# Optimization experiments

Measured on AMD Instinct MI355X. Metric: run time of the kernel, lower is better.

## Reference

```python
import jax, jax.numpy as jnp
import numpy as np

B, NPG = 32, 512            # graphs, nodes per graph
N = B * NPG                  # total nodes
EPG = 4096                   # edges per graph
E = B * EPG                  # total edges
H = 4                        # attention heads
IN, HID, OUT = 512, 128, 64
K1, K2 = 308, 185            # ceil(0.6*512), ceil(0.6*308) -- SAGPooling ratio=0.6
SLOPE = 0.2                  # GATv2 leaky_relu negative slope


def _segment_softmax(logit, seg, num_seg):
    # numerically stable softmax over edges grouped by destination node
    m = jax.ops.segment_max(logit, seg, num_segments=num_seg)
    m = jnp.where(jnp.isfinite(m), m, 0.0)
    ex = jnp.exp(logit - m[seg])
    s = jax.ops.segment_sum(ex, seg, num_segments=num_seg)
    return ex / (s[seg] + 1e-16)


def _gatv2(x, src, dst, valid, Wl, bl, Wr, br, att, bias, n):
    # PyG GATv2Conv, heads=H, concat=False (head-mean), add_self_loops=True,
    # attention dropout (0.2) is a no-op in eval mode.
    h, c = att.shape
    xl = (x @ Wl + bl).reshape(n, h, c)
    xr = (x @ Wr + br).reshape(n, h, c)
    loops = jnp.arange(n, dtype=src.dtype)
    sa = jnp.concatenate([src, loops])
    da = jnp.concatenate([dst, loops])
    va = jnp.concatenate([valid, jnp.ones((n,), bool)])
    seg = jnp.where(va, da, n)  # invalid edges -> dummy segment n
    e = jax.nn.leaky_relu(xl[sa] + xr[da], SLOPE)      # [Ea,h,c]
    logit = jnp.einsum('ehc,hc->eh', e, att)            # [Ea,h]
    alpha = _segment_softmax(logit, seg, n + 1)
    msg = alpha[:, :, None] * xl[sa]
    out = jax.ops.segment_sum(msg, seg, num_segments=n + 1)[:n]
    return out.mean(axis=1) + bias


def _sage_score(x, src, dst, valid, Wn, Wr, b, n):
    # PyG SAGEConv (mean aggr, root weight), out_channels=1 -> pooling score
    seg = jnp.where(valid, dst, n)
    vf = valid[:, None].astype(x.dtype)
    s = jax.ops.segment_sum(x[src] * vf, seg, num_segments=n + 1)[:n]
    cnt = jax.ops.segment_sum(valid.astype(x.dtype), seg, num_segments=n + 1)[:n]
    mean = s / jnp.maximum(cnt, 1.0)[:, None]
    return (mean @ Wn + x @ Wr + b).squeeze(-1)


def _pool(x, src, dst, valid, score, n_old, k):
    # SAGPooling top-k per graph (equal-sized graphs -> static k), tanh gating,
    # then filter_adj: keep edges whose endpoints both survive (mask + reindex).
    npg = n_old // B
    _, topi = jax.lax.top_k(score.reshape(B, npg), k)
    perm = (topi + (jnp.arange(B) * npg)[:, None]).reshape(-1)
    x_new = x[perm] * jnp.tanh(score[perm])[:, None]
    n_new = B * k
    nmap = jnp.full((n_old,), -1, src.dtype).at[perm].set(jnp.arange(n_new, dtype=src.dtype))
    ns, nd = nmap[src], nmap[dst]
    v = valid & (ns >= 0) & (nd >= 0)
    return x_new, jnp.where(v, ns, 0), jnp.where(v, nd, 0), v, n_new


def _gmp(x):
    # global max pool; nodes are grouped contiguously, equal count per graph
    return x.reshape(B, -1, x.shape[-1]).max(axis=1)


def _forward(x_feat, Wl1, bl1, Wr1, br1, att1, bias1,
             Wl2, bl2, Wr2, br2, att2, bias2,
             Wsn, Wsr, bs, Wf, bf, edge_index):
    src, dst = edge_index[0], edge_index[1]
    valid = jnp.ones((E,), bool)
    x = jax.nn.relu(_gatv2(x_feat, src, dst, valid, Wl1, bl1, Wr1, br1, att1, bias1, N))
    x1 = _gmp(x)
    sc = _sage_score(x, src, dst, valid, Wsn, Wsr, bs, N)
    x, s2, d2, v2, n2 = _pool(x, src, dst, valid, sc, N, K1)
    x2 = _gmp(x)
    x = jax.nn.relu(_gatv2(x, s2, d2, v2, Wl2, bl2, Wr2, br2, att2, bias2, n2))
    sc = _sage_score(x, s2, d2, v2, Wsn, Wsr, bs, n2)
    x, s3, d3, v3, n3 = _pool(x, s2, d2, v2, sc, n2, K2)
    x3 = _gmp(x)
    x = x1 + x2 + x3
    return jax.nn.relu(x @ Wf + bf)


def setup_inputs() -> dict:
    key = jax.random.key(0)
    ks = jax.random.split(key, 12)
    x_feat = jax.random.normal(ks[0], (N, IN), jnp.float32)
    sl = jax.random.randint(ks[1], (B, EPG), 0, NPG)
    dl = jax.random.randint(ks[2], (B, EPG), 0, NPG)
    off = (jnp.arange(B) * NPG)[:, None]
    edge_index = jnp.stack([(sl + off).reshape(-1), (dl + off).reshape(-1)])
    batch = jnp.repeat(jnp.arange(B), NPG)
    g = lambda k, shape, fan: jax.random.normal(k, shape, jnp.float32) / np.sqrt(fan).astype(np.float32)
    z = lambda shape: jnp.zeros(shape, jnp.float32)
    return dict(
        x_feat=x_feat, edge_index=edge_index, batch=batch,
        Wl1=g(ks[3], (IN, H * HID), IN), bl1=z((H * HID,)),
        Wr1=g(ks[4], (IN, H * HID), IN), br1=z((H * HID,)),
        att1=g(ks[5], (H, HID), HID), bias1=z((HID,)),
        Wl2=g(ks[6], (HID, H * HID), HID), bl2=z((H * HID,)),
        Wr2=g(ks[7], (HID, H * HID), HID), br2=z((H * HID,)),
        att2=g(ks[8], (H, HID), HID), bias2=z((HID,)),
        Wsn=g(ks[9], (HID, 1), HID), Wsr=g(ks[10], (HID, 1), HID), bs=z((1,)),
        Wf=g(ks[11], (HID, OUT), HID), bf=z((OUT,)),
    )


def reference(x_feat, edge_index, batch,
              Wl1, bl1, Wr1, br1, att1, bias1,
              Wl2, bl2, Wr2, br2, att2, bias2,
              Wsn, Wsr, bs, Wf, bf):
    # batch is implied by the contiguous equal-size grouping used above
    return _forward(x_feat, Wl1, bl1, Wr1, br1, att1, bias1,
                    Wl2, bl2, Wr2, br2, att2, bias2,
                    Wsn, Wsr, bs, Wf, bf, edge_index)
```

## Files before the change

### kernel.cpp

```cpp
#include <hip/hip_runtime.h>
#include <hip/hip_bf16.h>
#include <math.h>

#define NB    32
#define NPG   512
#define NTOT  (NB*NPG)
#define EPG   4096
#define ETOT  (NB*EPG)
#define K1    308
#define K2    185
#define N2    (NB*K1)
#define N3    (NB*K2)
#define SLOPE 0.2f

typedef _Float16 f16;
typedef f16   f16x8 __attribute__((ext_vector_type(8)));
typedef float f32x4 __attribute__((ext_vector_type(4)));

#define WSCALE 512.0f
#define WINV   (1.0f/512.0f)

__device__ __forceinline__ unsigned enc_f(float v) {
    unsigned u = __float_as_uint(v);
    return (u & 0x80000000u) ? ~u : (u | 0x80000000u);
}
__device__ __forceinline__ float dec_f(unsigned e) {
    return (e & 0x80000000u) ? __uint_as_float(e ^ 0x80000000u) : __uint_as_float(~e);
}

__device__ __forceinline__ void gll16(const void* g, void* l)
{
    __builtin_amdgcn_global_load_lds(
        (const __attribute__((address_space(1))) unsigned int*)g,
        (__attribute__((address_space(3))) unsigned int*)l, 16, 0, 0);
}


__global__ __launch_bounds__(256) void split_a(const float* __restrict__ A,
                                               f16* __restrict__ Ah, f16* __restrict__ Al,
                                               int K8, unsigned* __restrict__ xg,
                                               int* __restrict__ cnt)
{
    __shared__ float tile[64][65];
    int t = threadIdx.x;
    int kx = blockIdx.x, ry = blockIdx.y;
    int gid = (ry * gridDim.x + kx) * 256 + t;
    if (gid < 3 * NB * 128) xg[gid] = 0u;
    if (gid >= 16384 && gid < 16384 + NTOT + 8) cnt[gid - 16384] = 0;

    int K = K8 * 8;
    int r = t >> 2, q = t & 3;
    const float* src = A + (size_t)(ry * 64 + r) * K + kx * 64 + q * 16;
#pragma unroll
    for (int i = 0; i < 4; ++i) {
        float4 v = *(const float4*)(src + i * 4);
        tile[r][q * 16 + i * 4 + 0] = v.x;
        tile[r][q * 16 + i * 4 + 1] = v.y;
        tile[r][q * 16 + i * 4 + 2] = v.z;
        tile[r][q * 16 + i * 4 + 3] = v.w;
    }
    __syncthreads();
    int rr = t & 63, kb0 = t >> 6;
#pragma unroll
    for (int kk = 0; kk < 2; ++kk) {
        int kb = kb0 + kk * 4;
        f16x8 h, l;
#pragma unroll
        for (int c = 0; c < 8; ++c) {
            float v = tile[rr][kb * 8 + c];
            f16 hh = (f16)v;
            h[c] = hh;
            l[c] = (f16)(v - (float)hh);
        }
        size_t off = (((size_t)ry * K8 + kx * 8 + kb) * 64 + rr) * 8;
        *(f16x8*)(Ah + off) = h;
        *(f16x8*)(Al + off) = l;
    }
}

__global__ __launch_bounds__(256) void prep_w(const float* __restrict__ WL,
                                              const float* __restrict__ WR,
                                              f16* __restrict__ Wh, f16* __restrict__ Wlo,
                                              int K)
{
    __shared__ float t[32][33];
    int bk = blockIdx.x;
    int bn = blockIdx.y;
    int tx = threadIdx.x & 31, ty = threadIdx.x >> 5;
    const float* Wsrc = (bn < 16) ? WL : WR;
    int ncol = bn * 32 - (bn < 16 ? 0 : 512) + tx;
    int K8 = K >> 3;
#pragma unroll
    for (int q = 0; q < 4; ++q) {
        int kk = bk * 32 + ty + q * 8;
        t[ty + q * 8][tx] = Wsrc[(size_t)kk * 512 + ncol];
    }
    __syncthreads();
#pragma unroll
    for (int q = 0; q < 4; ++q) {
        int n = bn * 32 + ty + q * 8;
        int k = bk * 32 + tx;
        float v = t[tx][ty + q * 8] * WSCALE;
        f16 h = (f16)v;
        size_t off = (((size_t)(n >> 6) * K8 + (k >> 3)) * 64 + (n & 63)) * 8 + (k & 7);
        Wh [off] = h;
        Wlo[off] = (f16)(v - (float)h);
    }
}

__global__ __launch_bounds__(256) void gemm_split(
    const f16* __restrict__ Ah, const f16* __restrict__ Al,
    const f16* __restrict__ Bh, const f16* __restrict__ Bl,
    const float* __restrict__ bias_l, const float* __restrict__ bias_r,
    float* __restrict__ XL, float* __restrict__ XR, int M, int K)
{
    __shared__ f16 sm[2][4][4][128][8];
    int tid = threadIdx.x;
    int wave = tid >> 6, lane = tid & 63;

    int l = blockIdx.y * gridDim.x + blockIdx.x;
    int rows = gridDim.y;
    int row0 = (l % rows) * 128, col0 = (l / rows) * 128;

    const f16* base = (wave == 0) ? Ah : (wave == 1) ? Al : (wave == 2) ? Bh : Bl;
    int rc0 = (wave < 2) ? row0 : col0;
    int tr0 = rc0 >> 6;

    int wr = wave >> 1, wc = wave & 1;
    int r16 = lane & 15, kb = lane >> 4;

    const int K8 = K >> 3;
    const int nt = K >> 5;

    auto stage = [&](int buf, int t) {
#pragma unroll
        for (int i = 0; i < 8; ++i) {
            int kblk = i >> 1, rh = i & 1;
            const f16* src = base + ((((size_t)(tr0 + rh)) * K8 + (t * 4 + kblk)) << 9) + lane * 8;
            gll16(src, &sm[buf][wave][kblk][rh * 64][0]);
        }
    };

    f32x4 acc[4][4] = {};
    int cur = 0;
    stage(0, 0);

    for (int t = 0; t < nt; ++t) {
        if (t + 1 < nt) {
            stage(cur ^ 1, t + 1);
            asm volatile("s_waitcnt vmcnt(8)" ::: "memory");
        } else {
            asm volatile("s_waitcnt vmcnt(0)" ::: "memory");
        }
        __builtin_amdgcn_s_barrier();

        f16x8 a_h[4], a_l[4], b_h[4], b_l[4];
#pragma unroll
        for (int m = 0; m < 4; ++m) {
            a_h[m] = *(const f16x8*)&sm[cur][0][kb][wr * 64 + m * 16 + r16][0];
            a_l[m] = *(const f16x8*)&sm[cur][1][kb][wr * 64 + m * 16 + r16][0];
        }
#pragma unroll
        for (int n = 0; n < 4; ++n) {
            b_h[n] = *(const f16x8*)&sm[cur][2][kb][wc * 64 + n * 16 + r16][0];
            b_l[n] = *(const f16x8*)&sm[cur][3][kb][wc * 64 + n * 16 + r16][0];
        }
#pragma unroll
        for (int m = 0; m < 4; ++m)
#pragma unroll
            for (int n = 0; n < 4; ++n)
                acc[m][n] = __builtin_amdgcn_mfma_f32_16x16x32_f16(a_h[m], b_h[n], acc[m][n], 0, 0, 0);
#pragma unroll
        for (int m = 0; m < 4; ++m)
#pragma unroll
            for (int n = 0; n < 4; ++n)
                acc[m][n] = __builtin_amdgcn_mfma_f32_16x16x32_f16(a_h[m], b_l[n], acc[m][n], 0, 0, 0);
#pragma unroll
        for (int m = 0; m < 4; ++m)
#pragma unroll
            for (int n = 0; n < 4; ++n)
                acc[m][n] = __builtin_amdgcn_mfma_f32_16x16x32_f16(a_l[m], b_h[n], acc[m][n], 0, 0, 0);

        __syncthreads();
        cur ^= 1;
    }
    float* Co = (col0 < 512) ? XL : XR;
    const float* bo = (col0 < 512) ? bias_l : bias_r;
    int cbase = col0 - (col0 < 512 ? 0 : 512);
#pragma unroll
    for (int m = 0; m < 4; ++m)
#pragma unroll
        for (int n = 0; n < 4; ++n) {
            int cc = cbase + wc * 64 + n * 16 + r16;
            float b = bo[cc];
#pragma unroll
            for (int j = 0; j < 4; ++j) {
                int rr = row0 + wr * 64 + m * 16 + kb * 4 + j;
                Co[(size_t)rr * 512 + cc] = acc[m][n][j] * WINV + b;
            }
        }
}

__global__ void count_edges(const int* __restrict__ dst, int E_in, int* __restrict__ cnt)
{
    int e = blockIdx.x * blockDim.x + threadIdx.x;
    if (e < E_in) atomicAdd(&cnt[dst[e]], 1);
}

__global__ void fill_edges(const int* __restrict__ src, const int* __restrict__ dst,
                           int E_in, int* __restrict__ next, int* __restrict__ csr)
{
    int e = blockIdx.x * blockDim.x + threadIdx.x;
    if (e < E_in) {
        int p = atomicAdd(&next[dst[e]], 1);
        csr[p] = src[e];
    }
}

__global__ __launch_bounds__(512) void scan_graph(const int* __restrict__ cnt,
                                                  int* __restrict__ off, int* __restrict__ next)
{
    __shared__ int s[512];
    int g = blockIdx.x, t = threadIdx.x;
    int node = g * NPG + t;
    int v = cnt[node];
    s[t] = v;
    __syncthreads();
    for (int d = 1; d < 512; d <<= 1) {
        int u = (t >= d) ? s[t - d] : 0;
        __syncthreads();
        s[t] += u;
        __syncthreads();
    }
    int excl = s[t] - v + g * EPG;
    off[node] = excl;
    next[node] = excl;
    if (g == NB - 1 && t == 511) off[NTOT] = ETOT;
}

__global__ __launch_bounds__(64) void graph_sums(const int* __restrict__ cnt,
                                                 int* __restrict__ gsum)
{
    int b = blockIdx.x, t = threadIdx.x;
    int s = 0;
    for (int i = t; i < K1; i += 64) s += cnt[b * K1 + i];
#pragma unroll
    for (int sh = 1; sh < 64; sh <<= 1) s += __shfl_xor(s, sh);
    if (t == 0) gsum[b] = s;
}

__global__ __launch_bounds__(512) void scan_graph2(const int* __restrict__ cnt,
                                                   const int* __restrict__ gsum,
                                                   int* __restrict__ off, int* __restrict__ next)
{
    __shared__ int s[512];
    __shared__ int sbase;
    int b = blockIdx.x, t = threadIdx.x;
    if (t < 64) {
        int v = (t < b) ? gsum[t] : 0;
#pragma unroll
        for (int sh = 1; sh < 64; sh <<= 1) v += __shfl_xor(v, sh);
        if (t == 0) sbase = v;
    }
    int node = b * K1 + t;
    int c = (t < K1) ? cnt[node] : 0;
    s[t] = c;
    __syncthreads();
    for (int d = 1; d < 512; d <<= 1) {
        int u = (t >= d) ? s[t - d] : 0;
        __syncthreads();
        s[t] += u;
        __syncthreads();
    }
    int excl = sbase + s[t] - c;
    if (t < K1) { off[node] = excl; next[node] = excl; }
    if (b == NB - 1 && t == K1 - 1) off[N2] = excl + c;
}

__global__ void remap_edges(const int* __restrict__ src, const int* __restrict__ dst,
                            int E_in, const int* __restrict__ nmap,
                            int* __restrict__ es2, int* __restrict__ ed2,
                            int* __restrict__ ec2, int* __restrict__ cnt2)
{
    int e = blockIdx.x * blockDim.x + threadIdx.x;
    if (e >= E_in) return;
    int ns = nmap[src[e]], nd = nmap[dst[e]];
    if (ns >= 0 && nd >= 0) {
        int pos = atomicAdd(ec2, 1);
        es2[pos] = ns; ed2[pos] = nd;
        atomicAdd(&cnt2[nd], 1);
    }
}

__global__ void fill_edges_dyn(const int* __restrict__ es, const int* __restrict__ ed,
                               const int* __restrict__ ec, int* __restrict__ next,
                               int* __restrict__ csr)
{
    int e = blockIdx.x * blockDim.x + threadIdx.x;
    if (e < *ec) {
        int p = atomicAdd(&next[ed[e]], 1);
        csr[p] = es[e];
    }
}

__global__ __launch_bounds__(256) void gatv2_agg(
    const float* __restrict__ XL, const float* __restrict__ XR,
    const int* __restrict__ csr_src, const int* __restrict__ off,
    const float* __restrict__ att, const float* __restrict__ bias,
    const float* __restrict__ Wn, const float* __restrict__ Wr,
    float* __restrict__ out, float* __restrict__ y, float* __restrict__ z,
    int n, unsigned* __restrict__ xgOut, int npg, int* __restrict__ zc)
{
    __shared__ float hb[4][128];
    if (zc) {
        int raw = blockIdx.x * 256 + threadIdx.x;
        if (raw < NTOT + 2) zc[raw] = 0;
    }
    int nwg = gridDim.x;
    int q = nwg >> 3;
    int swz = (blockIdx.x & 7) * q + (blockIdx.x >> 3);
    int wv = threadIdx.x >> 6;
    int wid = swz * 4 + wv;
    int lane = threadIdx.x & 63;
    if (wid >= n) return;
    const int f0 = lane * 8;
    float xr[8], atv[8];
    {
        float4 r0 = *(const float4*)&XR[(size_t)wid * 512 + f0];
        float4 r1 = *(const float4*)&XR[(size_t)wid * 512 + f0 + 4];
        xr[0]=r0.x; xr[1]=r0.y; xr[2]=r0.z; xr[3]=r0.w;
        xr[4]=r1.x; xr[5]=r1.y; xr[6]=r1.z; xr[7]=r1.w;
        float4 t0 = *(const float4*)&att[f0];
        float4 t1 = *(const float4*)&att[f0 + 4];
        atv[0]=t0.x; atv[1]=t0.y; atv[2]=t0.z; atv[3]=t0.w;
        atv[4]=t1.x; atv[5]=t1.y; atv[6]=t1.z; atv[7]=t1.w;
    }

    auto loadrow = [&](int s, float* xl) {
        float4 l0 = *(const float4*)&XL[(size_t)s * 512 + f0];
        float4 l1 = *(const float4*)&XL[(size_t)s * 512 + f0 + 4];
        xl[0]=l0.x; xl[1]=l0.y; xl[2]=l0.z; xl[3]=l0.w;
        xl[4]=l1.x; xl[5]=l1.y; xl[6]=l1.z; xl[7]=l1.w;
    };
    auto logit = [&](const float* xl) {
        float part = 0.f;
#pragma unroll
        for (int j = 0; j < 8; ++j) {
            float v = xl[j] + xr[j];
            v = (v > 0.f) ? v : SLOPE * v;
            part += v * atv[j];
        }
        part += __shfl_xor(part, 1);
        part += __shfl_xor(part, 2);
        part += __shfl_xor(part, 4);
        part += __shfl_xor(part, 8);
        return part;
    };

    float xl0[8], acc[8];
    loadrow(wid, xl0);
    float m = logit(xl0), ssum = 1.f;
#pragma unroll
    for (int j = 0; j < 8; ++j) acc[j] = xl0[j];

    int e0 = off[wid], e1 = off[wid + 1];
    int e = e0;
    for (; e + 3 < e1; e += 4) {
        int s1 = csr_src[e], s2 = csr_src[e + 1], s3 = csr_src[e + 2], s4 = csr_src[e + 3];
        float xl1[8], xl2[8], xl3[8], xl4[8];
        loadrow(s1, xl1);
        loadrow(s2, xl2);
        loadrow(s3, xl3);
        loadrow(s4, xl4);
        float p1 = logit(xl1), p2 = logit(xl2), p3 = logit(xl3), p4 = logit(xl4);
        float mx = fmaxf(fmaxf(p1, p2), fmaxf(p3, p4));
        float mn = fmaxf(m, mx);
        float scale = __expf(m - mn);
        float q1 = __expf(p1 - mn), q2 = __expf(p2 - mn);
        float q3 = __expf(p3 - mn), q4 = __expf(p4 - mn);
        ssum = ssum * scale + (q1 + q2 + q3 + q4);
#pragma unroll
        for (int j = 0; j < 8; ++j)
            acc[j] = acc[j] * scale + (q1 * xl1[j] + q2 * xl2[j] + q3 * xl3[j] + q4 * xl4[j]);
        m = mn;
    }
    for (; e < e1; ++e) {
        int s1 = csr_src[e];
        float xl1[8];
        loadrow(s1, xl1);
        float p1 = logit(xl1);
        float mn = fmaxf(m, p1);
        float scale = __expf(m - mn);
        float q1 = __expf(p1 - mn);
        ssum = ssum * scale + q1;
#pragma unroll
        for (int j = 0; j < 8; ++j) acc[j] = acc[j] * scale + q1 * xl1[j];
        m = mn;
    }

    float inv = 1.f / ssum;
    float py = 0.f, pz = 0.f;
#pragma unroll
    for (int j = 0; j < 8; ++j) {
        float v = acc[j] * inv;
        v += __shfl_xor(v, 16);
        v += __shfl_xor(v, 32);
        if (lane < 16) {
            int c = lane * 8 + j;
            float r = fmaxf(0.25f * v + bias[c], 0.f);
            out[(size_t)wid * 128 + c] = r;
            py += r * Wn[c];
            pz += r * Wr[c];
            if (xgOut) hb[wv][c] = r;
        }
    }
#pragma unroll
    for (int sh = 1; sh < 16; sh <<= 1) {
        py += __shfl_xor(py, sh);
        pz += __shfl_xor(pz, sh);
    }
    if (lane == 0) { y[wid] = py; z[wid] = pz; }
    if (xgOut) {
        __syncthreads();
        int t = threadIdx.x;
        if (t < 128) {
            float mx = fmaxf(fmaxf(hb[0][t], hb[1][t]), fmaxf(hb[2][t], hb[3][t]));
            int gb = (swz * 4) / npg;
            atomicMax(&xgOut[gb * 128 + t], enc_f(mx));
        }
    }
}

__global__ __launch_bounds__(512) void sage_rank(
    const float* __restrict__ y, const float* __restrict__ z,
    const int* __restrict__ csr, const int* __restrict__ off,
    const float* __restrict__ bs, int npg, int k,
    float* __restrict__ score, int* __restrict__ nmap)
{
    __shared__ float s[512];
    int b = blockIdx.x, t = threadIdx.x;
    int node = b * npg + t;
    if (t < npg) {
        int e0 = off[node], e1 = off[node + 1];
        float a = 0.f;
        int e = e0;
        for (; e + 3 < e1; e += 4)
            a += y[csr[e]] + y[csr[e + 1]] + y[csr[e + 2]] + y[csr[e + 3]];
        for (; e < e1; ++e) a += y[csr[e]];
        float sc = a / fmaxf((float)(e1 - e0), 1.f) + z[node] + bs[0];
        s[t] = sc;
        score[node] = sc;
    }
    __syncthreads();
    if (t < npg) {
        float mine = s[t];
        int rank = 0;
        for (int j = 0; j < npg; ++j) {
            float v = s[j];
            rank += (v > mine) || (v == mine && j < t);
        }
        nmap[node] = (rank < k) ? (b * k + rank) : -1;
    }
}

__global__ __launch_bounds__(256) void pool_gather(
    const float* __restrict__ X, const float* __restrict__ score,
    const int* __restrict__ nmap, f16* __restrict__ Xh, f16* __restrict__ Xl,
    unsigned* __restrict__ xgOut, int kk, int ntot)
{
    int gid = blockIdx.x * 256 + threadIdx.x;
    int i = gid >> 6, l6 = gid & 63;
    if (i >= ntot) return;
    int nid = nmap[i];
    if (nid < 0) return;
    int c0 = l6 * 2;
    float t = tanhf(score[i]);
    float2 xv = *(const float2*)&X[(size_t)i * 128 + c0];
    float v0 = xv.x * t, v1 = xv.y * t;
    if (Xh) {
        size_t off = (((size_t)(nid >> 6) * 16 + (c0 >> 3)) * 64 + (nid & 63)) * 8 + (c0 & 7);
        f16 h0 = (f16)v0, h1 = (f16)v1;
        Xh[off] = h0;     Xl[off] = (f16)(v0 - (float)h0);
        Xh[off + 1] = h1; Xl[off + 1] = (f16)(v1 - (float)h1);
    }
    int b = nid / kk;
    atomicMax(&xgOut[b * 128 + c0], enc_f(v0));
    atomicMax(&xgOut[b * 128 + c0 + 1], enc_f(v1));
}

__global__ void final_mlp(const unsigned* __restrict__ xg,
                          const float* __restrict__ Wf,
                          const float* __restrict__ bf, float* __restrict__ out)
{
    int b = blockIdx.x, o = threadIdx.x;
    float acc = bf[o];
    for (int c = 0; c < 128; ++c) {
        int i = b * 128 + c;
        float xv = dec_f(xg[i]) + dec_f(xg[4096 + i]) + dec_f(xg[8192 + i]);
        acc += xv * Wf[c * 64 + o];
    }
    out[b * 64 + o] = fmaxf(acc, 0.f);
}

static inline size_t alignup(size_t x) { return (x + 255) & ~(size_t)255; }

extern "C" void kernel_launch(void* const* d_in, const int* in_sizes, int n_in,
                              void* d_out, int out_size, void* d_ws, size_t ws_size,
                              hipStream_t stream)
{
    const float* x_feat = (const float*)d_in[0];
    const int*   ei     = (const int*)d_in[1];
    const float* Wl1  = (const float*)d_in[3];
    const float* bl1  = (const float*)d_in[4];
    const float* Wr1  = (const float*)d_in[5];
    const float* br1  = (const float*)d_in[6];
    const float* att1 = (const float*)d_in[7];
    const float* bias1= (const float*)d_in[8];
    const float* Wl2  = (const float*)d_in[9];
    const float* bl2  = (const float*)d_in[10];
    const float* Wr2  = (const float*)d_in[11];
    const float* br2  = (const float*)d_in[12];
    const float* att2 = (const float*)d_in[13];
    const float* bias2= (const float*)d_in[14];
    const float* Wsn  = (const float*)d_in[15];
    const float* Wsr  = (const float*)d_in[16];
    const float* bs   = (const float*)d_in[17];
    const float* Wf   = (const float*)d_in[18];
    const float* bf   = (const float*)d_in[19];
    float* out = (float*)d_out;

    const int* e_src = ei;
    const int* e_dst = ei + ETOT;

    char* ws = (char*)d_ws;
    size_t o = 0;
    auto take = [&](size_t bytes) { size_t r = o; o = alignup(o + bytes); return r; };
    float* XL   = (float*)(ws + take((size_t)NTOT * 512 * 4));
    float* XR   = (float*)(ws + take((size_t)NTOT * 512 * 4));
    float* H1   = (float*)(ws + take((size_t)NTOT * 128 * 4));
    float* H2   = (float*)(ws + take((size_t)N2 * 128 * 4));
    f16*   Ah1  = (f16*)(ws + take((size_t)NTOT * 512 * 2));
    f16*   Al1  = (f16*)(ws + take((size_t)NTOT * 512 * 2));
    f16*   Wh1  = (f16*)(ws + take((size_t)1024 * 512 * 2));
    f16*   Wo1  = (f16*)(ws + take((size_t)1024 * 512 * 2));
    f16*   Wh2  = (f16*)(ws + take((size_t)1024 * 128 * 2));
    f16*   Wo2  = (f16*)(ws + take((size_t)1024 * 128 * 2));
    f16*   PXh  = (f16*)(ws + take((size_t)N2 * 128 * 2));
    f16*   PXl  = (f16*)(ws + take((size_t)N2 * 128 * 2));
    float* score= (float*)(ws + take((size_t)NTOT * 4));
    float* yb   = (float*)(ws + take((size_t)NTOT * 4));
    float* zb   = (float*)(ws + take((size_t)NTOT * 4));
    int*   nmap = (int*)(ws + take((size_t)NTOT * 4));
    int*   cnt  = (int*)(ws + take((size_t)(NTOT + 1) * 4 + 256));
    int*   offs = (int*)(ws + take((size_t)(NTOT + 1) * 4));
    int*   nxt  = (int*)(ws + take((size_t)(NTOT + 1) * 4));
    int*   gsum = (int*)(ws + take(256));
    int*   csr1 = (int*)(ws + take((size_t)ETOT * 4));
    int*   es2  = (int*)(ws + take((size_t)ETOT * 4));
    int*   ed2  = (int*)(ws + take((size_t)ETOT * 4));
    int*   csr2 = (int*)(ws + take((size_t)ETOT * 4));
    unsigned* xg = (unsigned*)(ws + take((size_t)3 * NB * 128 * 4));
    int* ec2 = cnt + NTOT + 1;
    (void)ws_size; (void)in_sizes; (void)n_in; (void)out_size;

    split_a<<<dim3(8, NTOT / 64), 256, 0, stream>>>(x_feat, Ah1, Al1, 64, xg, cnt);
    prep_w<<<dim3(512 / 32, 32), 256, 0, stream>>>(Wl1, Wr1, Wh1, Wo1, 512);
    prep_w<<<dim3(128 / 32, 32), 256, 0, stream>>>(Wl2, Wr2, Wh2, Wo2, 128);

    gemm_split<<<dim3(8, NTOT / 128), 256, 0, stream>>>(Ah1, Al1, Wh1, Wo1, bl1, br1, XL, XR, NTOT, 512);

    count_edges<<<ETOT / 256, 256, 0, stream>>>(e_dst, ETOT, cnt);
    scan_graph<<<NB, 512, 0, stream>>>(cnt, offs, nxt);
    fill_edges<<<ETOT / 256, 256, 0, stream>>>(e_src, e_dst, ETOT, nxt, csr1);

    gatv2_agg<<<NTOT / 4, 256, 0, stream>>>(XL, XR, csr1, offs, att1, bias1, Wsn, Wsr,
                                            H1, yb, zb, NTOT, xg, NPG, cnt);

    sage_rank<<<NB, 512, 0, stream>>>(yb, zb, csr1, offs, bs, NPG, K1, score, nmap);
    pool_gather<<<NTOT * 64 / 256, 256, 0, stream>>>(H1, score, nmap, PXh, PXl, xg + 4096, K1, NTOT);

    remap_edges<<<ETOT / 256, 256, 0, stream>>>(e_src, e_dst, ETOT, nmap, es2, ed2, ec2, cnt);
    graph_sums<<<NB, 64, 0, stream>>>(cnt, gsum);
    scan_graph2<<<NB, 512, 0, stream>>>(cnt, gsum, offs, nxt);
    fill_edges_dyn<<<ETOT / 256, 256, 0, stream>>>(es2, ed2, ec2, nxt, csr2);

    gemm_split<<<dim3(8, N2 / 128), 256, 0, stream>>>(PXh, PXl, Wh2, Wo2, bl2, br2, XL, XR, N2, 128);

    gatv2_agg<<<(N2 + 3) / 4, 256, 0, stream>>>(XL, XR, csr2, offs, att2, bias2, Wsn, Wsr,
                                                H2, yb, zb, N2, (unsigned*)nullptr, K1, (int*)nullptr);

    sage_rank<<<NB, 512, 0, stream>>>(yb, zb, csr2, offs, bs, K1, K2, score, nmap);
    pool_gather<<<(N2 * 64 + 255) / 256, 256, 0, stream>>>(H2, score, nmap, (f16*)nullptr, (f16*)nullptr,
                                                           xg + 8192, K2, N2);

    final_mlp<<<NB, 64, 0, stream>>>(xg, Wf, bf, out);
}
```

Baseline: 296.5 us.

## Fuse pooling rank with gather, merge weight prep and second-stage scan kernels

Merges the SAGPooling ranking and gather/tanh-gating/max-readout into one per-graph kernel that computes the graph max in shared memory instead of global atomics. Also combines the two weight-prep launches into one 3D grid and folds the graph-sum step into the second scan. It adds nontemporal loads/stores in the GATv2 aggregation. This reduces launch count and atomic traffic, but the fused pool kernel uses only one block per graph, lowering parallelism for the gather.

```diff
diff --git a/kernel.cpp b/kernel.cpp
--- a/kernel.cpp
+++ b/kernel.cpp
@@ -16,6 +16,7 @@
 typedef _Float16 f16;
 typedef f16   f16x8 __attribute__((ext_vector_type(8)));
 typedef float f32x4 __attribute__((ext_vector_type(4)));
+typedef float fv4   __attribute__((ext_vector_type(4)));
 
 #define WSCALE 512.0f
 #define WINV   (1.0f/512.0f)
@@ -78,11 +79,20 @@
     }
 }
 
-__global__ __launch_bounds__(256) void prep_w(const float* __restrict__ WL,
-                                              const float* __restrict__ WR,
-                                              f16* __restrict__ Wh, f16* __restrict__ Wlo,
-                                              int K)
-{
+__global__ __launch_bounds__(256) void prep_w_all(
+    const float* __restrict__ WL1, const float* __restrict__ WR1,
+    f16* __restrict__ Wh1, f16* __restrict__ Wo1,
+    const float* __restrict__ WL2, const float* __restrict__ WR2,
+    f16* __restrict__ Wh2, f16* __restrict__ Wo2)
+{
+    int zi = blockIdx.z;
+    if (zi == 1 && blockIdx.x >= 4) return;
+    const float* WL = zi ? WL2 : WL1;
+    const float* WR = zi ? WR2 : WR1;
+    f16* Wh  = zi ? Wh2 : Wh1;
+    f16* Wlo = zi ? Wo2 : Wo1;
+    int K = zi ? 128 : 512;
+
     __shared__ float t[32][33];
     int bk = blockIdx.x;
     int bn = blockIdx.y;
@@ -238,30 +248,22 @@
     if (g == NB - 1 && t == 511) off[NTOT] = ETOT;
 }
 
-__global__ __launch_bounds__(64) void graph_sums(const int* __restrict__ cnt,
-                                                 int* __restrict__ gsum)
-{
+__global__ __launch_bounds__(512) void scan2_fused(const int* __restrict__ cnt,
+                                                   int* __restrict__ off, int* __restrict__ next)
+{
+    __shared__ int s[512];
+    __shared__ int base_s;
     int b = blockIdx.x, t = threadIdx.x;
-    int s = 0;
-    for (int i = t; i < K1; i += 64) s += cnt[b * K1 + i];
-#pragma unroll
-    for (int sh = 1; sh < 64; sh <<= 1) s += __shfl_xor(s, sh);
-    if (t == 0) gsum[b] = s;
-}
-
-__global__ __launch_bounds__(512) void scan_graph2(const int* __restrict__ cnt,
-                                                   const int* __restrict__ gsum,
-                                                   int* __restrict__ off, int* __restrict__ next)
-{
-    __shared__ int s[512];
-    __shared__ int sbase;
-    int b = blockIdx.x, t = threadIdx.x;
-    if (t < 64) {
-        int v = (t < b) ? gsum[t] : 0;
-#pragma unroll
-        for (int sh = 1; sh < 64; sh <<= 1) v += __shfl_xor(v, sh);
-        if (t == 0) sbase = v;
-    }
+    int pre = 0;
+    for (int i = t; i < b * K1; i += 512) pre += cnt[i];
+    s[t] = pre;
+    __syncthreads();
+    for (int d = 256; d > 0; d >>= 1) {
+        if (t < d) s[t] += s[t + d];
+        __syncthreads();
+    }
+    if (t == 0) base_s = s[0];
+    __syncthreads();
     int node = b * K1 + t;
     int c = (t < K1) ? cnt[node] : 0;
     s[t] = c;
@@ -272,7 +274,7 @@
         s[t] += u;
         __syncthreads();
     }
-    int excl = sbase + s[t] - c;
+    int excl = base_s + s[t] - c;
     if (t < K1) { off[node] = excl; next[node] = excl; }
     if (b == NB - 1 && t == K1 - 1) off[N2] = excl + c;
 }
@@ -326,8 +328,8 @@
     const int f0 = lane * 8;
     float xr[8], atv[8];
     {
-        float4 r0 = *(const float4*)&XR[(size_t)wid * 512 + f0];
-        float4 r1 = *(const float4*)&XR[(size_t)wid * 512 + f0 + 4];
+        fv4 r0 = __builtin_nontemporal_load((const fv4*)&XR[(size_t)wid * 512 + f0]);
+        fv4 r1 = __builtin_nontemporal_load((const fv4*)&XR[(size_t)wid * 512 + f0 + 4]);
         xr[0]=r0.x; xr[1]=r0.y; xr[2]=r0.z; xr[3]=r0.w;
         xr[4]=r1.x; xr[5]=r1.y; xr[6]=r1.z; xr[7]=r1.w;
         float4 t0 = *(const float4*)&att[f0];
@@ -408,7 +410,7 @@
         if (lane < 16) {
             int c = lane * 8 + j;
             float r = fmaxf(0.25f * v + bias[c], 0.f);
-            out[(size_t)wid * 128 + c] = r;
+            __builtin_nontemporal_store(r, &out[(size_t)wid * 128 + c]);
             py += r * Wn[c];
             pz += r * Wr[c];
             if (xgOut) hb[wv][c] = r;
@@ -431,16 +433,21 @@
     }
 }
 
-__global__ __launch_bounds__(512) void sage_rank(
+__global__ __launch_bounds__(512) void sage_rank_pool(
     const float* __restrict__ y, const float* __restrict__ z,
     const int* __restrict__ csr, const int* __restrict__ off,
     const float* __restrict__ bs, int npg, int k,
-    float* __restrict__ score, int* __restrict__ nmap)
+    const float* __restrict__ H, int* __restrict__ nmap_out,
+    f16* __restrict__ Xh, f16* __restrict__ Xl, unsigned* __restrict__ xgOut)
 {
     __shared__ float s[512];
+    __shared__ float gate[512];
+    __shared__ int   rl[512];
+    __shared__ float bmax[4][128];
     int b = blockIdx.x, t = threadIdx.x;
-    int node = b * npg + t;
+    int node0 = b * npg;
     if (t < npg) {
+        int node = node0 + t;
         int e0 = off[node], e1 = off[node + 1];
         float a = 0.f;
         int e = e0;
@@ -449,7 +456,7 @@
         for (; e < e1; ++e) a += y[csr[e]];
         float sc = a / fmaxf((float)(e1 - e0), 1.f) + z[node] + bs[0];
         s[t] = sc;
-        score[node] = sc;
+        gate[t] = tanhf(sc);
     }
     __syncthreads();
     if (t < npg) {
@@ -459,33 +466,31 @@
             float v = s[j];
             rank += (v > mine) || (v == mine && j < t);
         }
-        nmap[node] = (rank < k) ? (b * k + rank) : -1;
-    }
-}
-
-__global__ __launch_bounds__(256) void pool_gather(
-    const float* __restrict__ X, const float* __restrict__ score,
-    const int* __restrict__ nmap, f16* __restrict__ Xh, f16* __restrict__ Xl,
-    unsigned* __restrict__ xgOut, int kk, int ntot)
-{
-    int gid = blockIdx.x * 256 + threadIdx.x;
-    int i = gid >> 6, l6 = gid & 63;
-    if (i >= ntot) return;
-    int nid = nmap[i];
-    if (nid < 0) return;
-    int c0 = l6 * 2;
-    float t = tanhf(score[i]);
-    float2 xv = *(const float2*)&X[(size_t)i * 128 + c0];
-    float v0 = xv.x * t, v1 = xv.y * t;
-    if (Xh) {
-        size_t off = (((size_t)(nid >> 6) * 16 + (c0 >> 3)) * 64 + (nid & 63)) * 8 + (c0 & 7);
-        f16 h0 = (f16)v0, h1 = (f16)v1;
-        Xh[off] = h0;     Xl[off] = (f16)(v0 - (float)h0);
-        Xh[off + 1] = h1; Xl[off + 1] = (f16)(v1 - (float)h1);
-    }
-    int b = nid / kk;
-    atomicMax(&xgOut[b * 128 + c0], enc_f(v0));
-    atomicMax(&xgOut[b * 128 + c0 + 1], enc_f(v1));
+        int nid = (rank < k) ? (b * k + rank) : -1;
+        rl[t] = nid;
+        if (nmap_out) nmap_out[node0 + t] = nid;
+    }
+    __syncthreads();
+    int ch = t & 127, sub = t >> 7;
+    float mx = -INFINITY;
+    for (int nl = sub; nl < npg; nl += 4) {
+        int nid = rl[nl];
+        if (nid < 0) continue;
+        float v = H[(size_t)(node0 + nl) * 128 + ch] * gate[nl];
+        mx = fmaxf(mx, v);
+        if (Xh) {
+            size_t o = (((size_t)(nid >> 6) * 16 + (ch >> 3)) * 64 + (nid & 63)) * 8 + (ch & 7);
+            f16 h = (f16)v;
+            Xh[o] = h;
+            Xl[o] = (f16)(v - (float)h);
+        }
+    }
+    bmax[sub][ch] = mx;
+    __syncthreads();
+    if (t < 128) {
+        float m4 = fmaxf(fmaxf(bmax[0][t], bmax[1][t]), fmaxf(bmax[2][t], bmax[3][t]));
+        xgOut[b * 128 + t] = enc_f(m4);
+    }
 }
 
 __global__ void final_mlp(const unsigned* __restrict__ xg,
@@ -547,14 +552,12 @@
     f16*   Wo2  = (f16*)(ws + take((size_t)1024 * 128 * 2));
     f16*   PXh  = (f16*)(ws + take((size_t)N2 * 128 * 2));
     f16*   PXl  = (f16*)(ws + take((size_t)N2 * 128 * 2));
-    float* score= (float*)(ws + take((size_t)NTOT * 4));
     float* yb   = (float*)(ws + take((size_t)NTOT * 4));
     float* zb   = (float*)(ws + take((size_t)NTOT * 4));
     int*   nmap = (int*)(ws + take((size_t)NTOT * 4));
     int*   cnt  = (int*)(ws + take((size_t)(NTOT + 1) * 4 + 256));
     int*   offs = (int*)(ws + take((size_t)(NTOT + 1) * 4));
     int*   nxt  = (int*)(ws + take((size_t)(NTOT + 1) * 4));
-    int*   gsum = (int*)(ws + take(256));
     int*   csr1 = (int*)(ws + take((size_t)ETOT * 4));
     int*   es2  = (int*)(ws + take((size_t)ETOT * 4));
     int*   ed2  = (int*)(ws + take((size_t)ETOT * 4));
@@ -564,8 +567,7 @@
     (void)ws_size; (void)in_sizes; (void)n_in; (void)out_size;
 
     split_a<<<dim3(8, NTOT / 64), 256, 0, stream>>>(x_feat, Ah1, Al1, 64, xg, cnt);
-    prep_w<<<dim3(512 / 32, 32), 256, 0, stream>>>(Wl1, Wr1, Wh1, Wo1, 512);
-    prep_w<<<dim3(128 / 32, 32), 256, 0, stream>>>(Wl2, Wr2, Wh2, Wo2, 128);
+    prep_w_all<<<dim3(16, 32, 2), 256, 0, stream>>>(Wl1, Wr1, Wh1, Wo1, Wl2, Wr2, Wh2, Wo2);
 
     gemm_split<<<dim3(8, NTOT / 128), 256, 0, stream>>>(Ah1, Al1, Wh1, Wo1, bl1, br1, XL, XR, NTOT, 512);
 
@@ -576,12 +578,11 @@
     gatv2_agg<<<NTOT / 4, 256, 0, stream>>>(XL, XR, csr1, offs, att1, bias1, Wsn, Wsr,
                                             H1, yb, zb, NTOT, xg, NPG, cnt);
 
-    sage_rank<<<NB, 512, 0, stream>>>(yb, zb, csr1, offs, bs, NPG, K1, score, nmap);
-    pool_gather<<<NTOT * 64 / 256, 256, 0, stream>>>(H1, score, nmap, PXh, PXl, xg + 4096, K1, NTOT);
+    sage_rank_pool<<<NB, 512, 0, stream>>>(yb, zb, csr1, offs, bs, NPG, K1,
+                                           H1, nmap, PXh, PXl, xg + 4096);
 
     remap_edges<<<ETOT / 256, 256, 0, stream>>>(e_src, e_dst, ETOT, nmap, es2, ed2, ec2, cnt);
-    graph_sums<<<NB, 64, 0, stream>>>(cnt, gsum);
-    scan_graph2<<<NB, 512, 0, stream>>>(cnt, gsum, offs, nxt);
+    scan2_fused<<<NB, 512, 0, stream>>>(cnt, offs, nxt);
     fill_edges_dyn<<<ETOT / 256, 256, 0, stream>>>(es2, ed2, ec2, nxt, csr2);
 
     gemm_split<<<dim3(8, N2 / 128), 256, 0, stream>>>(PXh, PXl, Wh2, Wo2, bl2, br2, XL, XR, N2, 128);
@@ -589,9 +590,8 @@
     gatv2_agg<<<(N2 + 3) / 4, 256, 0, stream>>>(XL, XR, csr2, offs, att2, bias2, Wsn, Wsr,
                                                 H2, yb, zb, N2, (unsigned*)nullptr, K1, (int*)nullptr);
 
-    sage_rank<<<NB, 512, 0, stream>>>(yb, zb, csr2, offs, bs, K1, K2, score, nmap);
-    pool_gather<<<(N2 * 64 + 255) / 256, 256, 0, stream>>>(H2, score, nmap, (f16*)nullptr, (f16*)nullptr,
-                                                           xg + 8192, K2, N2);
+    sage_rank_pool<<<NB, 512, 0, stream>>>(yb, zb, csr2, offs, bs, K1, K2,
+                                           H2, (int*)nullptr, (f16*)nullptr, (f16*)nullptr, xg + 8192);
 
     final_mlp<<<NB, 64, 0, stream>>>(xg, Wf, bf, out);
 }
```

Result: slower. 324.4 us (+9.4%).
